# Performance work log

Measured on AMD Instinct MI355X. Metric: run time of the kernel, lower is better.

The kernel has to match this reference:

```python
import jax, jax.numpy as jnp
import numpy as np

B, S, D, H = 2, 2048, 256, 8

def setup_inputs() -> dict:
    key = jax.random.key(0)
    ks = jax.random.split(key, 7)
    inputs = jax.random.normal(ks[0], (B, S, D), dtype=jnp.float32)
    timestamp = jnp.sort(jax.random.randint(ks[1], (B, S), 0, 100000, dtype=jnp.int32), axis=-1)
    wQ = jax.random.normal(ks[2], (H, D, D), dtype=jnp.float32) * 0.05
    wK = jax.random.normal(ks[3], (H, D, D), dtype=jnp.float32) * 0.05
    wV = jax.random.normal(ks[4], (H, D, D), dtype=jnp.float32) * 0.05
    wO = jax.random.normal(ks[5], (H * D, D), dtype=jnp.float32) * 0.05
    theta = jax.random.uniform(ks[6], (1, 1), dtype=jnp.float32)
    return {"inputs": inputs, "timestamp": timestamp, "wQ": wQ, "wK": wK,
            "wV": wV, "wO": wO, "theta": theta}

def reference(inputs, timestamp, wQ, wK, wV, wO, theta):
    b, s, d = inputs.shape
    # per-head projections (original loops over heads via TensorArray; vectorized here)
    Q = jnp.einsum('bsd,hde->bhse', inputs, wQ)
    K = jnp.einsum('bsd,hde->bhse', inputs, wK)
    V = jnp.einsum('bsd,hde->bhse', inputs, wV)
    exp_x = jnp.einsum('bhsd,bhtd->bhst', Q, K) / jnp.sqrt(jnp.float32(d))  # [B,H,S,S]
    x = jax.nn.softmax(exp_x, axis=-1)
    low_tri = jnp.tril(jnp.ones((s, s), dtype=jnp.float32))
    x = x * low_tri
    x = x / jnp.sum(x, axis=-1, keepdims=True)  # causal renormalized softmax

    # time-decay double-softmax branch. NOTE: the original module computes `a`
    # but returns x @ V, so `a`/`s_`/`d_` do not affect the output (dead code,
    # reproduced here for fidelity; XLA will DCE it).
    ts = timestamp.astype(jnp.float32)
    d_t = ts[:, None, :, None] - ts[:, None, None, :]  # diag(t) - t : [B,1,S,S]
    decay = (1.0 - jnp.cumsum(x, axis=-1)) * d_t * low_tri
    s_ = exp_x * jnp.exp(-(theta[0, 0] * theta[0, 0]) * decay)
    a = jax.nn.softmax(s_, axis=-1) * low_tri
    a = a / jnp.sum(a, axis=-1, keepdims=True)
    del a  # unused in original output

    ret = jnp.einsum('bhst,bhtd->bhsd', x, V)          # [B,H,S,D]
    out = ret.transpose(0, 2, 1, 3).reshape(b, s, -1)  # concat heads -> [B,S,H*D]
    return out @ wO
```

## Files before the change

kernel.cpp:

```cpp
#include <hip/hip_runtime.h>
#include <cstdint>
#include <cstddef>

#define S_LEN 2048
#define DIM   256
#define NH    8
#define NB    2
#define HDIM  (NH * DIM)

using bf16 = __bf16;
typedef __bf16 bf16x8 __attribute__((ext_vector_type(8)));
typedef __bf16 bf16x4 __attribute__((ext_vector_type(4)));
typedef float  f32x4  __attribute__((ext_vector_type(4)));

typedef const __attribute__((address_space(1))) unsigned int* as1_u32p;
typedef __attribute__((address_space(3))) unsigned int* as3_u32p;

__device__ __forceinline__ void cp16(const bf16* g, bf16* l) {
    __builtin_amdgcn_global_load_lds((as1_u32p)g, (as3_u32p)l, 16, 0, 0);
}

__global__ __launch_bounds__(256) void prep_kernel(const float* __restrict__ X,
                                                   const float* __restrict__ wQ,
                                                   const float* __restrict__ wK,
                                                   const float* __restrict__ wV,
                                                   const float* __restrict__ wO,
                                                   bf16* __restrict__ Xb,
                                                   bf16* __restrict__ WQt,
                                                   bf16* __restrict__ WKt,
                                                   bf16* __restrict__ WVt,
                                                   bf16* __restrict__ WOt)
{
    const int z = blockIdx.z;
    if (z == 4) {
        const int t = (blockIdx.y*4 + blockIdx.x)*256 + threadIdx.x;
        #pragma unroll
        for (int p = 0; p < 8; ++p) {
            const int i = (t + p*32768)*4;
            float4 v = *(const float4*)(X + i);
            bf16x4 o;
            o[0] = (bf16)v.x; o[1] = (bf16)v.y; o[2] = (bf16)v.z; o[3] = (bf16)v.w;
            *(bf16x4*)(Xb + i) = o;
        }
        return;
    }
    __shared__ float tile[64][65];
    const float* in; bf16* out; int R, C, r0, c0;
    if (z < 3) {
        const int h = blockIdx.y >> 2;
        in  = (z == 0 ? wQ : z == 1 ? wK : wV) + (size_t)h * DIM * DIM;
        out = (z == 0 ? WQt : z == 1 ? WKt : WVt) + (size_t)h * DIM * DIM;
        R = DIM; C = DIM; r0 = (blockIdx.y & 3) * 64; c0 = blockIdx.x * 64;
    } else {
        in = wO; out = WOt; R = HDIM; C = DIM;
        r0 = blockIdx.y * 64; c0 = blockIdx.x * 64;
    }
    const int tr  = threadIdx.x >> 4;
    const int tc4 = (threadIdx.x & 15) * 4;
    #pragma unroll
    for (int p = 0; p < 4; ++p) {
        int row = p * 16 + tr;
        float4 v = *(const float4*)(in + (size_t)(r0 + row) * C + c0 + tc4);
        tile[row][tc4+0] = v.x; tile[row][tc4+1] = v.y;
        tile[row][tc4+2] = v.z; tile[row][tc4+3] = v.w;
    }
    __syncthreads();
    #pragma unroll
    for (int p = 0; p < 4; ++p) {
        int orow = p * 16 + tr;
        bf16x4 o;
        #pragma unroll
        for (int j = 0; j < 4; ++j) o[j] = (bf16)tile[tc4 + j][orow];
        *(bf16x4*)(out + (size_t)(c0 + orow) * R + r0 + tc4) = o;
    }
}

template<int EPI>
__device__ __forceinline__ void gemm_tile(const bf16* __restrict__ A, const bf16* __restrict__ BT,
                                          void* __restrict__ C, bf16* As, bf16* Bs,
                                          int tm, int tn, int K, int lda, int ldb, int ldc)
{
    const int tid  = threadIdx.x;
    const int lane = tid & 63;
    const int wave = tid >> 6;
    const int wm   = (wave >> 1) << 6;
    const int wn   = (wave & 1) << 6;
    const int l16  = lane & 15;
    const int quad = lane >> 4;

    const int m0 = tm << 7, n0 = tn << 7;

    const int srow = (lane >> 2);
    const int gch  = (lane & 3) ^ (srow & 3);

    f32x4 acc[4][4] = {};

    const int ksteps = K >> 5;

    #pragma unroll
    for (int j = 0; j < 2; ++j) {
        const int g = wave*2 + j;
        cp16(A  + (size_t)(m0 + g*16 + srow)*lda + (gch << 3), As + g*512);
        cp16(BT + (size_t)(n0 + g*16 + srow)*ldb + (gch << 3), Bs + g*512);
    }

    for (int ks = 0; ks < ksteps; ++ks) {
        const int pb = ks & 1;
        asm volatile("s_waitcnt vmcnt(0)" ::: "memory");
        __syncthreads();
        if (ks + 1 < ksteps) {
            const int k1 = (ks + 1) << 5;
            #pragma unroll
            for (int j = 0; j < 2; ++j) {
                const int g = wave*2 + j;
                cp16(A  + (size_t)(m0 + g*16 + srow)*lda + k1 + (gch << 3),
                     As + (pb ^ 1)*4096 + g*512);
                cp16(BT + (size_t)(n0 + g*16 + srow)*ldb + k1 + (gch << 3),
                     Bs + (pb ^ 1)*4096 + g*512);
            }
        }
        const bf16* Ab = As + pb*4096;
        const bf16* Bb = Bs + pb*4096;
        bf16x8 af[4], bfv[4];
        #pragma unroll
        for (int i = 0; i < 4; ++i) {
            const int row = wm + i*16 + l16;
            af[i]  = *(const bf16x8*)(Ab + row*32 + ((quad ^ (l16 & 3)) << 3));
        }
        #pragma unroll
        for (int i = 0; i < 4; ++i) {
            const int row = wn + i*16 + l16;
            bfv[i] = *(const bf16x8*)(Bb + row*32 + ((quad ^ (l16 & 3)) << 3));
        }
        #pragma unroll
        for (int i = 0; i < 4; ++i)
            #pragma unroll
            for (int j = 0; j < 4; ++j)
                acc[i][j] = __builtin_amdgcn_mfma_f32_16x16x32_bf16(af[i], bfv[j], acc[i][j], 0, 0, 0);
    }

    #pragma unroll
    for (int i = 0; i < 4; ++i)
        #pragma unroll
        for (int j = 0; j < 4; ++j)
            #pragma unroll
            for (int r = 0; r < 4; ++r) {
                int mg = m0 + wm + i*16 + quad*4 + r;
                int ng = n0 + wn + j*16 + l16;
                float v = acc[i][j][r];
                if (EPI == 0)      ((bf16*)C)[(size_t)mg * ldc + ng] = (bf16)v;
                else if (EPI == 1) ((float*)C)[(size_t)mg * ldc + ng] = v;
                else               atomicAdd(&((float*)C)[(size_t)mg * ldc + ng], v);
            }
}

__global__ __launch_bounds__(256) void proj_kernel(const bf16* __restrict__ Xb,
    const bf16* __restrict__ WQt, const bf16* __restrict__ WKt, const bf16* __restrict__ WVt,
    bf16* __restrict__ Qg, bf16* __restrict__ Kg, bf16* __restrict__ VTg)
{
    __shared__ __align__(16) bf16 smem[4 * 4096];
    const int by  = blockIdx.y;
    const int mat = by >> 4;
    const int b   = (by >> 3) & 1;
    const int h   = by & 7;
    const int bx  = blockIdx.x;
    const bf16*  Xbb = Xb + (size_t)b * S_LEN * DIM;
    const size_t bh  = (size_t)(b * NH + h);
    if (mat == 0) {
        gemm_tile<0>(Xbb, WQt + (size_t)h*DIM*DIM, Qg + bh*S_LEN*DIM, smem, smem + 8192,
                     bx & 15, bx >> 4, DIM, DIM, DIM, DIM);
    } else if (mat == 1) {
        gemm_tile<0>(Xbb, WKt + (size_t)h*DIM*DIM, Kg + bh*S_LEN*DIM, smem, smem + 8192,
                     bx & 15, bx >> 4, DIM, DIM, DIM, DIM);
    } else {
        gemm_tile<0>(WVt + (size_t)h*DIM*DIM, Xbb, VTg + bh*DIM*S_LEN, smem, smem + 8192,
                     bx & 1, bx >> 1, DIM, DIM, DIM, S_LEN);
    }
}

__global__ __launch_bounds__(256) void outproj_kernel(const bf16* __restrict__ Ret,
                                                      const bf16* __restrict__ WOt,
                                                      float* __restrict__ out)
{
    __shared__ __align__(16) bf16 smem[4 * 4096];
    int bx = blockIdx.x;
    int t  = bx & 63;
    int kq = bx >> 6;
    gemm_tile<2>(Ret + kq*512, WOt + kq*512, out, smem, smem + 8192,
                 t >> 1, t & 1, 512, HDIM, HDIM, DIM);
}

__global__ __launch_bounds__(256) void attn_kernel(const bf16* __restrict__ Qg,
                                                   const bf16* __restrict__ Kg,
                                                   const bf16* __restrict__ VTg,
                                                   bf16* __restrict__ Ret,
                                                   bf16* __restrict__ Opart,
                                                   float* __restrict__ Lpart)
{
    __shared__ __align__(16) bf16 KsB[2][32 * 256];
    __shared__ __align__(16) bf16 VTs[256 * 32];
    __shared__ __align__(16) bf16 Ps [4 * 16 * 40];

    static const unsigned char order[63] = {
        10,31,32,60, 29,30,57,58,61,62, 9,27,28,51,54,55,56,59,
        25,26,48,49,52,53, 8,23,24,42,45,46,47,50, 21,22,39,40,43,44,
        7,19,20,33,36,37,38,41, 17,18,34,35, 6,15,16, 13,14, 5,11,12,
        4,3,2,1,0 };

    const int tid  = threadIdx.x;
    const int lane = tid & 63;
    const int wave = tid >> 6;
    const int l16  = lane & 15;
    const int quad = lane >> 4;

    const int bx  = blockIdx.x;
    const int bh  = bx & 15;
    const int bid = order[bx >> 4];
    int qt, s, nsp;
    if (bid <= 10)      { qt = bid;              s = 0;       nsp = 1; }
    else if (bid <= 32) { int k = bid - 11; qt = 11 + (k >> 1); s = k & 1; nsp = 2; }
    else                { int k = bid - 33; int q3 = k / 3; qt = 22 + q3; s = k - 3*q3; nsp = 3; }
    const int b = bh >> 3, h = bh & 7;

    int kstep0, kstep1;
    if (nsp == 1)      { kstep0 = 0; kstep1 = 2*qt + 2; }
    else if (nsp == 2) { kstep0 = s*(qt + 1); kstep1 = kstep0 + qt + 1; }
    else {
        const int S2 = 2*qt + 2, base = S2/3, rem = S2 - 3*base;
        kstep0 = s*base + (s < rem ? s : rem);
        kstep1 = kstep0 + base + (s < rem ? 1 : 0);
    }

    const bf16* Qbh  = Qg  + (size_t)(b*NH + h) * S_LEN * DIM;
    const bf16* Kbh  = Kg  + (size_t)(b*NH + h) * S_LEN * DIM;
    const bf16* VTbh = VTg + (size_t)(b*NH + h) * DIM * S_LEN;

    const int qbase = qt * 64 + wave * 16;

    bf16x8 qf[8];
    #pragma unroll
    for (int kc = 0; kc < 8; ++kc)
        qf[kc] = *(const bf16x8*)(Qbh + (size_t)(qbase + l16)*DIM + kc*32 + quad*8);

    f32x4 o[16] = {};
    float l_part[4] = {0.f, 0.f, 0.f, 0.f};

    {
        const int t00 = kstep0 << 5;
        #pragma unroll
        for (int j = 0; j < 4; ++j) {
            const int sN = (((wave << 2) + j) << 6) + lane;
            const int ts = sN >> 5, cs = sN & 31;
            cp16(Kbh + (size_t)(t00 + ts)*DIM + ((cs ^ ts) << 3),
                 &KsB[0][0] + (((wave << 2) + j) << 9));
        }
    }

    for (int step = kstep0; step < kstep1; ++step) {
        const int pb = (step - kstep0) & 1;
        asm volatile("s_waitcnt vmcnt(0)\n\ts_barrier" ::: "memory");

        const int t0 = step << 5;
        #pragma unroll
        for (int j = 0; j < 4; ++j) {
            const int sN = (((wave << 2) + j) << 6) + lane;
            const int es = sN >> 2, cs = sN & 3;
            cp16(VTbh + (size_t)es*S_LEN + t0 + ((cs ^ ((es >> 1) & 3)) << 3),
                 &VTs[0] + (((wave << 2) + j) << 9));
        }
        const bool havek = (step + 1 < kstep1);
        if (havek) {
            const int t1 = (step + 1) << 5;
            #pragma unroll
            for (int j = 0; j < 4; ++j) {
                const int sN = (((wave << 2) + j) << 6) + lane;
                const int ts = sN >> 5, cs = sN & 31;
                cp16(Kbh + (size_t)(t1 + ts)*DIM + ((cs ^ ts) << 3),
                     &KsB[pb ^ 1][0] + (((wave << 2) + j) << 9));
            }
        }

        const bf16* KsP = &KsB[pb][0];

        f32x4 sacc[2] = {};
        #pragma unroll
        for (int kc = 0; kc < 8; ++kc) {
            const int ch = (kc << 2) + quad;
            bf16x8 b0 = *(const bf16x8*)(KsP + (l16 << 8)        + ((ch ^ l16) << 3));
            bf16x8 b1 = *(const bf16x8*)(KsP + ((16 + l16) << 8) + ((ch ^ (16 + l16)) << 3));
            sacc[0] = __builtin_amdgcn_mfma_f32_16x16x32_bf16(qf[kc], b0, sacc[0], 0,0,0);
            sacc[1] = __builtin_amdgcn_mfma_f32_16x16x32_bf16(qf[kc], b1, sacc[1], 0,0,0);
        }

        float pv[2][4];
        #pragma unroll
        for (int r2 = 0; r2 < 4; ++r2) {
            const int qgi = qbase + quad*4 + r2;
            const bool ok0 = (t0 + l16)      <= qgi;
            const bool ok1 = (t0 + 16 + l16) <= qgi;
            float p0 = ok0 ? __expf(sacc[0][r2] * 0.0625f) : 0.0f;
            float p1 = ok1 ? __expf(sacc[1][r2] * 0.0625f) : 0.0f;
            l_part[r2] += p0 + p1;
            pv[0][r2] = p0; pv[1][r2] = p1;
        }

        #pragma unroll
        for (int nt = 0; nt < 2; ++nt)
            #pragma unroll
            for (int r2 = 0; r2 < 4; ++r2)
                Ps[wave*640 + (quad*4 + r2)*40 + nt*16 + l16] = (bf16)pv[nt][r2];

        if (havek) asm volatile("s_waitcnt vmcnt(4)\n\ts_barrier" ::: "memory");
        else       asm volatile("s_waitcnt vmcnt(0)\n\ts_barrier" ::: "memory");

        bf16x8 pf = *(const bf16x8*)(Ps + wave*640 + l16*40 + quad*8);
        #pragma unroll
        for (int ct = 0; ct < 16; ++ct) {
            const int e = (ct << 4) + l16;
            bf16x8 vf = *(const bf16x8*)(&VTs[0] + (e << 5) + ((quad ^ ((e >> 1) & 3)) << 3));
            o[ct] = __builtin_amdgcn_mfma_f32_16x16x32_bf16(pf, vf, o[ct], 0,0,0);
        }
    }

    float lsum[4];
    #pragma unroll
    for (int r2 = 0; r2 < 4; ++r2) {
        float l = l_part[r2];
        l += __shfl_xor(l, 1);
        l += __shfl_xor(l, 2);
        l += __shfl_xor(l, 4);
        l += __shfl_xor(l, 8);
        lsum[r2] = l;
    }

    if (nsp == 1) {
        #pragma unroll
        for (int r2 = 0; r2 < 4; ++r2) {
            const int qgi = qbase + quad*4 + r2;
            const float inv = 1.0f / lsum[r2];
            #pragma unroll
            for (int ct = 0; ct < 16; ++ct)
                Ret[((size_t)b*S_LEN + qgi)*HDIM + h*DIM + ct*16 + l16] = (bf16)(o[ct][r2] * inv);
        }
    } else {
        const int slotbase = (qt <= 21) ? ((qt - 11)*2 + s) : (22 + (qt - 22)*3 + s);
        const size_t slot = (size_t)bh*52 + slotbase;
        bf16*  Ob = Opart + slot * (64*256);
        float* Lb = Lpart + slot * 64;
        #pragma unroll
        for (int r2 = 0; r2 < 4; ++r2) {
            const int trow = wave*16 + quad*4 + r2;
            #pragma unroll
            for (int ct = 0; ct < 16; ++ct)
                Ob[(size_t)trow*256 + ct*16 + l16] = (bf16)o[ct][r2];
            if (l16 == 0) Lb[trow] = lsum[r2];
        }
    }
}

__global__ __launch_bounds__(256) void combine_kernel(const bf16* __restrict__ Opart,
                                                      const float* __restrict__ Lpart,
                                                      bf16* __restrict__ Ret)
{
    const int bx = blockIdx.x;
    const int bh = bx / 21;
    const int ti = bx - bh*21;
    const int qt = 11 + ti;
    const int n  = (qt <= 21) ? 2 : 3;
    const int slotbase = (qt <= 21) ? (qt - 11)*2 : (22 + (qt - 22)*3);
    const size_t slot0 = (size_t)bh*52 + slotbase;
    const int b = bh >> 3, h = bh & 7;
    const int row  = threadIdx.x >> 2;
    const int col0 = (threadIdx.x & 3) * 64;

    float l = 0.f;
    for (int i = 0; i < n; ++i) l += Lpart[(slot0 + i)*64 + row];
    const float inv = 1.0f / l;

    const bf16* O0 = Opart + slot0 * (64*256) + (size_t)row*256 + col0;
    const int q = qt*64 + row;
    bf16* dst = Ret + ((size_t)b*S_LEN + q)*HDIM + h*DIM + col0;
    #pragma unroll
    for (int ch = 0; ch < 8; ++ch) {
        float acc[8] = {};
        for (int i = 0; i < n; ++i) {
            bf16x8 a = *(const bf16x8*)(O0 + (size_t)i*(64*256) + ch*8);
            #pragma unroll
            for (int j = 0; j < 8; ++j) acc[j] += (float)a[j];
        }
        bf16x8 w;
        #pragma unroll
        for (int j = 0; j < 8; ++j) w[j] = (bf16)(acc[j] * inv);
        *(bf16x8*)(dst + ch*8) = w;
    }
}


extern "C" void kernel_launch(void* const* d_in, const int* in_sizes, int n_in,
                              void* d_out, int out_size, void* d_ws, size_t ws_size,
                              hipStream_t stream)
{
    (void)in_sizes; (void)n_in; (void)ws_size;
    const float* X  = (const float*)d_in[0];
    const float* wQ = (const float*)d_in[2];
    const float* wK = (const float*)d_in[3];
    const float* wV = (const float*)d_in[4];
    const float* wO = (const float*)d_in[5];

    char* ws = (char*)d_ws;
    const size_t MB = 1u << 20;
    bf16*  Xb    = (bf16*)(ws + 0*MB);
    bf16*  WQt   = (bf16*)(ws + 2*MB);
    bf16*  WKt   = (bf16*)(ws + 3*MB);
    bf16*  WVt   = (bf16*)(ws + 4*MB);
    bf16*  WOt   = (bf16*)(ws + 5*MB);
    bf16*  Qg    = (bf16*)(ws + 6*MB);
    bf16*  Kg    = (bf16*)(ws + 22*MB);
    bf16*  VTg   = (bf16*)(ws + 38*MB);
    bf16*  Ret   = (bf16*)(ws + 54*MB);
    bf16*  Opart = (bf16*)(ws + 70*MB);
    float* Lpart = (float*)(ws + 98*MB);

    hipMemsetAsync(d_out, 0, (size_t)out_size * sizeof(float), stream);

    prep_kernel    <<<dim3(4, 32, 5), 256, 0, stream>>>(X, wQ, wK, wV, wO,
                                                        Xb, WQt, WKt, WVt, WOt);
    proj_kernel    <<<dim3(32, 48), 256, 0, stream>>>(Xb, WQt, WKt, WVt, Qg, Kg, VTg);
    attn_kernel    <<<1008,         256, 0, stream>>>(Qg, Kg, VTg, Ret, Opart, Lpart);
    combine_kernel <<<336,          256, 0, stream>>>(Opart, Lpart, Ret);
    outproj_kernel <<<256,          256, 0, stream>>>(Ret, WOt, (float*)d_out);
}
```

Before: 198.0 us.

## Restructure attention kernel to 64-wide key tiles with 32x32x16 MFMA

The attention kernel now processes 64 keys per step instead of 32 and switches from 16x16x32 to 32x32x16 MFMA tiles. A 2x2 wave layout splits query rows and key/output columns, partial row sums are combined through shared memory, and K is single-buffered with the next tile prefetched after the P write. The goal is fewer loop iterations and barriers and more operand reuse per MFMA. The cost is larger LDS use, more registers, a request for two blocks per CU, and less overlap of K loads with compute.

```diff
diff --git a/kernel.cpp b/kernel.cpp
--- a/kernel.cpp
+++ b/kernel.cpp
@@ -12,6 +12,7 @@
 typedef __bf16 bf16x8 __attribute__((ext_vector_type(8)));
 typedef __bf16 bf16x4 __attribute__((ext_vector_type(4)));
 typedef float  f32x4  __attribute__((ext_vector_type(4)));
+typedef float  f32x16 __attribute__((ext_vector_type(16)));
 
 typedef const __attribute__((address_space(1))) unsigned int* as1_u32p;
 typedef __attribute__((address_space(3))) unsigned int* as3_u32p;
@@ -190,170 +191,180 @@
                  t >> 1, t & 1, 512, HDIM, HDIM, DIM);
 }
 
-__global__ __launch_bounds__(256) void attn_kernel(const bf16* __restrict__ Qg,
-                                                   const bf16* __restrict__ Kg,
-                                                   const bf16* __restrict__ VTg,
-                                                   bf16* __restrict__ Ret,
-                                                   bf16* __restrict__ Opart,
-                                                   float* __restrict__ Lpart)
-{
-    __shared__ __align__(16) bf16 KsB[2][32 * 256];
-    __shared__ __align__(16) bf16 VTs[256 * 32];
-    __shared__ __align__(16) bf16 Ps [4 * 16 * 40];
+__global__ __launch_bounds__(256, 2) void attn_kernel(const bf16* __restrict__ Qg,
+                                                      const bf16* __restrict__ Kg,
+                                                      const bf16* __restrict__ VTg,
+                                                      bf16* __restrict__ Ret,
+                                                      bf16* __restrict__ Opart,
+                                                      float* __restrict__ Lpart)
+{
+    __shared__ __align__(16) bf16 Ks [64 * 256];
+    __shared__ __align__(16) bf16 VTs[256 * 64];
+    __shared__ __align__(16) bf16 Ps [64 * 72];
 
     static const unsigned char order[63] = {
-        10,31,32,60, 29,30,57,58,61,62, 9,27,28,51,54,55,56,59,
-        25,26,48,49,52,53, 8,23,24,42,45,46,47,50, 21,22,39,40,43,44,
-        7,19,20,33,36,37,38,41, 17,18,34,35, 6,15,16, 13,14, 5,11,12,
+        10,29,31,32,57,60,61,
+        9,25,27,28,30,48,51,52,54,55,56,58,59,62,
+        8,21,23,24,26,39,42,43,45,46,47,49,50,53,
+        7,17,19,20,22,33,34,36,37,38,40,41,44,
+        6,13,15,16,18,35,
+        5,11,12,14,
         4,3,2,1,0 };
 
     const int tid  = threadIdx.x;
     const int lane = tid & 63;
     const int wave = tid >> 6;
-    const int l16  = lane & 15;
-    const int quad = lane >> 4;
+    const int l32  = lane & 31;
+    const int half = lane >> 5;
+    const int rh   = wave >> 1;
+    const int kh   = wave & 1;
+    const int cw   = (wave & 1) * 128;
 
     const int bx  = blockIdx.x;
     const int bh  = bx & 15;
     const int bid = order[bx >> 4];
     int qt, s, nsp;
-    if (bid <= 10)      { qt = bid;              s = 0;       nsp = 1; }
+    if (bid <= 10)      { qt = bid;                    s = 0;       nsp = 1; }
     else if (bid <= 32) { int k = bid - 11; qt = 11 + (k >> 1); s = k & 1; nsp = 2; }
     else                { int k = bid - 33; int q3 = k / 3; qt = 22 + q3; s = k - 3*q3; nsp = 3; }
     const int b = bh >> 3, h = bh & 7;
 
-    int kstep0, kstep1;
-    if (nsp == 1)      { kstep0 = 0; kstep1 = 2*qt + 2; }
-    else if (nsp == 2) { kstep0 = s*(qt + 1); kstep1 = kstep0 + qt + 1; }
-    else {
-        const int S2 = 2*qt + 2, base = S2/3, rem = S2 - 3*base;
-        kstep0 = s*base + (s < rem ? s : rem);
-        kstep1 = kstep0 + base + (s < rem ? 1 : 0);
-    }
+    const int S2 = qt + 1;
+    const int base = S2 / nsp, rem = S2 - nsp*base;
+    const int kstep0 = s*base + (s < rem ? s : rem);
+    const int kstep1 = kstep0 + base + (s < rem ? 1 : 0);
 
     const bf16* Qbh  = Qg  + (size_t)(b*NH + h) * S_LEN * DIM;
     const bf16* Kbh  = Kg  + (size_t)(b*NH + h) * S_LEN * DIM;
     const bf16* VTbh = VTg + (size_t)(b*NH + h) * DIM * S_LEN;
 
-    const int qbase = qt * 64 + wave * 16;
-
-    bf16x8 qf[8];
-    #pragma unroll
-    for (int kc = 0; kc < 8; ++kc)
-        qf[kc] = *(const bf16x8*)(Qbh + (size_t)(qbase + l16)*DIM + kc*32 + quad*8);
-
-    f32x4 o[16] = {};
-    float l_part[4] = {0.f, 0.f, 0.f, 0.f};
+    const int qbase32 = qt*64 + rh*32;
+
+    bf16x8 qf[16];
+    #pragma unroll
+    for (int kc = 0; kc < 16; ++kc)
+        qf[kc] = *(const bf16x8*)(Qbh + (size_t)(qbase32 + l32)*DIM + kc*16 + half*8);
+
+    f32x16 o[4] = {};
+    float l_part[16] = {};
 
     {
-        const int t00 = kstep0 << 5;
-        #pragma unroll
-        for (int j = 0; j < 4; ++j) {
-            const int sN = (((wave << 2) + j) << 6) + lane;
+        const int t00 = kstep0 << 6;
+        #pragma unroll
+        for (int j = 0; j < 8; ++j) {
+            const int sN = ((wave*8 + j) << 6) + lane;
             const int ts = sN >> 5, cs = sN & 31;
-            cp16(Kbh + (size_t)(t00 + ts)*DIM + ((cs ^ ts) << 3),
-                 &KsB[0][0] + (((wave << 2) + j) << 9));
+            cp16(Kbh + (size_t)(t00 + ts)*DIM + ((cs ^ (ts & 31)) << 3),
+                 Ks + ((wave*8 + j) << 9));
         }
     }
 
     for (int step = kstep0; step < kstep1; ++step) {
-        const int pb = (step - kstep0) & 1;
-        asm volatile("s_waitcnt vmcnt(0)\n\ts_barrier" ::: "memory");
-
-        const int t0 = step << 5;
-        #pragma unroll
-        for (int j = 0; j < 4; ++j) {
-            const int sN = (((wave << 2) + j) << 6) + lane;
-            const int es = sN >> 2, cs = sN & 3;
-            cp16(VTbh + (size_t)es*S_LEN + t0 + ((cs ^ ((es >> 1) & 3)) << 3),
-                 &VTs[0] + (((wave << 2) + j) << 9));
-        }
-        const bool havek = (step + 1 < kstep1);
-        if (havek) {
-            const int t1 = (step + 1) << 5;
-            #pragma unroll
-            for (int j = 0; j < 4; ++j) {
-                const int sN = (((wave << 2) + j) << 6) + lane;
+        const int t0 = step << 6;
+        asm volatile("s_barrier" ::: "memory");
+        #pragma unroll
+        for (int j = 0; j < 8; ++j) {
+            const int sN = ((wave*8 + j) << 6) + lane;
+            const int es = sN >> 3, cs = sN & 7;
+            cp16(VTbh + (size_t)es*S_LEN + t0 + ((cs ^ (es & 7)) << 3),
+                 VTs + ((wave*8 + j) << 9));
+        }
+        asm volatile("s_waitcnt vmcnt(8)\n\ts_barrier" ::: "memory");
+
+        f32x16 sacc = {};
+        #pragma unroll
+        for (int kc = 0; kc < 16; ++kc) {
+            const int g = kc*2 + half;
+            bf16x8 kf = *(const bf16x8*)(Ks + (size_t)(kh*32 + l32)*256 + ((g ^ l32) << 3));
+            sacc = __builtin_amdgcn_mfma_f32_32x32x16_bf16(qf[kc], kf, sacc, 0, 0, 0);
+        }
+
+        const int tg = t0 + kh*32 + l32;
+        #pragma unroll
+        for (int r = 0; r < 16; ++r) {
+            const int lrow = rh*32 + 4*half + (r & 3) + 8*(r >> 2);
+            const int qgi  = qt*64 + lrow;
+            float p = (tg <= qgi) ? __expf(sacc[r] * 0.0625f) : 0.0f;
+            l_part[r] += p;
+            Ps[lrow*72 + kh*32 + l32] = (bf16)p;
+        }
+
+        __syncthreads();
+
+        if (step + 1 < kstep1) {
+            const int t1 = (step + 1) << 6;
+            #pragma unroll
+            for (int j = 0; j < 8; ++j) {
+                const int sN = ((wave*8 + j) << 6) + lane;
                 const int ts = sN >> 5, cs = sN & 31;
-                cp16(Kbh + (size_t)(t1 + ts)*DIM + ((cs ^ ts) << 3),
-                     &KsB[pb ^ 1][0] + (((wave << 2) + j) << 9));
+                cp16(Kbh + (size_t)(t1 + ts)*DIM + ((cs ^ (ts & 31)) << 3),
+                     Ks + ((wave*8 + j) << 9));
             }
         }
 
-        const bf16* KsP = &KsB[pb][0];
-
-        f32x4 sacc[2] = {};
-        #pragma unroll
-        for (int kc = 0; kc < 8; ++kc) {
-            const int ch = (kc << 2) + quad;
-            bf16x8 b0 = *(const bf16x8*)(KsP + (l16 << 8)        + ((ch ^ l16) << 3));
-            bf16x8 b1 = *(const bf16x8*)(KsP + ((16 + l16) << 8) + ((ch ^ (16 + l16)) << 3));
-            sacc[0] = __builtin_amdgcn_mfma_f32_16x16x32_bf16(qf[kc], b0, sacc[0], 0,0,0);
-            sacc[1] = __builtin_amdgcn_mfma_f32_16x16x32_bf16(qf[kc], b1, sacc[1], 0,0,0);
-        }
-
-        float pv[2][4];
-        #pragma unroll
-        for (int r2 = 0; r2 < 4; ++r2) {
-            const int qgi = qbase + quad*4 + r2;
-            const bool ok0 = (t0 + l16)      <= qgi;
-            const bool ok1 = (t0 + 16 + l16) <= qgi;
-            float p0 = ok0 ? __expf(sacc[0][r2] * 0.0625f) : 0.0f;
-            float p1 = ok1 ? __expf(sacc[1][r2] * 0.0625f) : 0.0f;
-            l_part[r2] += p0 + p1;
-            pv[0][r2] = p0; pv[1][r2] = p1;
-        }
-
-        #pragma unroll
-        for (int nt = 0; nt < 2; ++nt)
-            #pragma unroll
-            for (int r2 = 0; r2 < 4; ++r2)
-                Ps[wave*640 + (quad*4 + r2)*40 + nt*16 + l16] = (bf16)pv[nt][r2];
-
-        if (havek) asm volatile("s_waitcnt vmcnt(4)\n\ts_barrier" ::: "memory");
-        else       asm volatile("s_waitcnt vmcnt(0)\n\ts_barrier" ::: "memory");
-
-        bf16x8 pf = *(const bf16x8*)(Ps + wave*640 + l16*40 + quad*8);
-        #pragma unroll
-        for (int ct = 0; ct < 16; ++ct) {
-            const int e = (ct << 4) + l16;
-            bf16x8 vf = *(const bf16x8*)(&VTs[0] + (e << 5) + ((quad ^ ((e >> 1) & 3)) << 3));
-            o[ct] = __builtin_amdgcn_mfma_f32_16x16x32_bf16(pf, vf, o[ct], 0,0,0);
-        }
-    }
-
-    float lsum[4];
-    #pragma unroll
-    for (int r2 = 0; r2 < 4; ++r2) {
-        float l = l_part[r2];
+        bf16x8 pf[4];
+        #pragma unroll
+        for (int kc = 0; kc < 4; ++kc)
+            pf[kc] = *(const bf16x8*)(Ps + (rh*32 + l32)*72 + kc*16 + half*8);
+        #pragma unroll
+        for (int ct = 0; ct < 4; ++ct) {
+            f32x16 acc = o[ct];
+            #pragma unroll
+            for (int kc = 0; kc < 4; ++kc) {
+                const int e = cw + ct*32 + l32;
+                const int g = kc*2 + half;
+                bf16x8 vf = *(const bf16x8*)(VTs + (size_t)e*64 + ((g ^ (e & 7)) << 3));
+                acc = __builtin_amdgcn_mfma_f32_32x32x16_bf16(pf[kc], vf, acc, 0, 0, 0);
+            }
+            o[ct] = acc;
+        }
+    }
+
+    #pragma unroll
+    for (int r = 0; r < 16; ++r) {
+        float l = l_part[r];
         l += __shfl_xor(l, 1);
         l += __shfl_xor(l, 2);
         l += __shfl_xor(l, 4);
         l += __shfl_xor(l, 8);
-        lsum[r2] = l;
-    }
+        l += __shfl_xor(l, 16);
+        l_part[r] = l;
+    }
+
+    __syncthreads();
+    float* Lp = (float*)Ps;
+    if (l32 == 0) {
+        #pragma unroll
+        for (int r = 0; r < 16; ++r) {
+            const int lrow = rh*32 + 4*half + (r & 3) + 8*(r >> 2);
+            Lp[kh*64 + lrow] = l_part[r];
+        }
+    }
+    __syncthreads();
 
     if (nsp == 1) {
         #pragma unroll
-        for (int r2 = 0; r2 < 4; ++r2) {
-            const int qgi = qbase + quad*4 + r2;
-            const float inv = 1.0f / lsum[r2];
-            #pragma unroll
-            for (int ct = 0; ct < 16; ++ct)
-                Ret[((size_t)b*S_LEN + qgi)*HDIM + h*DIM + ct*16 + l16] = (bf16)(o[ct][r2] * inv);
+        for (int r = 0; r < 16; ++r) {
+            const int lrow = rh*32 + 4*half + (r & 3) + 8*(r >> 2);
+            const float inv = 1.0f / (Lp[lrow] + Lp[64 + lrow]);
+            const int qgi = qt*64 + lrow;
+            #pragma unroll
+            for (int ct = 0; ct < 4; ++ct)
+                Ret[((size_t)b*S_LEN + qgi)*HDIM + h*DIM + cw + ct*32 + l32]
+                    = (bf16)(o[ct][r] * inv);
         }
     } else {
         const int slotbase = (qt <= 21) ? ((qt - 11)*2 + s) : (22 + (qt - 22)*3 + s);
         const size_t slot = (size_t)bh*52 + slotbase;
         bf16*  Ob = Opart + slot * (64*256);
         float* Lb = Lpart + slot * 64;
-        #pragma unroll
-        for (int r2 = 0; r2 < 4; ++r2) {
-            const int trow = wave*16 + quad*4 + r2;
-            #pragma unroll
-            for (int ct = 0; ct < 16; ++ct)
-                Ob[(size_t)trow*256 + ct*16 + l16] = (bf16)o[ct][r2];
-            if (l16 == 0) Lb[trow] = lsum[r2];
+        if (tid < 64) Lb[tid] = Lp[tid] + Lp[64 + tid];
+        #pragma unroll
+        for (int r = 0; r < 16; ++r) {
+            const int lrow = rh*32 + 4*half + (r & 3) + 8*(r >> 2);
+            #pragma unroll
+            for (int ct = 0; ct < 4; ++ct)
+                Ob[(size_t)lrow*256 + cw + ct*32 + l32] = (bf16)o[ct][r];
         }
     }
 }
```

Result: slower. 236.3 us (+19.4%).
